# Kernel tuning notes

Hardware: AMD Instinct MI355X
Metric: run time of the kernel (lower is better)

Reference implementation:

```python
import jax, jax.numpy as jnp
from jax import lax
import numpy as np

B, QLEN, HQ, HKV, D, MAXLEN = 16, 1, 32, 8, 128, 8192
END_INDEX = 4096


def setup_inputs() -> dict:
    key = jax.random.key(0)
    k1, k2, k3, k4, k5 = jax.random.split(key, 5)
    query = jax.random.normal(k1, (B, QLEN, HQ, D), dtype=jnp.float32)
    new_key = jax.random.normal(k2, (B, QLEN, HKV, D), dtype=jnp.float32)
    new_value = jax.random.normal(k3, (B, QLEN, HKV, D), dtype=jnp.float32)
    key_cache = jax.random.normal(k4, (B, MAXLEN, HKV, D), dtype=jnp.float32)
    value_cache = jax.random.normal(k5, (B, MAXLEN, HKV, D), dtype=jnp.float32)
    attention_mask = jnp.ones((B, MAXLEN), dtype=jnp.bool_)
    # standard lower-triangular causal mask, (1, 1, L, L)
    causal_mask = jnp.tril(jnp.ones((MAXLEN, MAXLEN), dtype=jnp.bool_))[None, None]
    return {
        "query": query,
        "key": new_key,
        "value": new_value,
        "key_cache": key_cache,
        "value_cache": value_cache,
        "attention_mask": attention_mask,
        "causal_mask": causal_mask,
        "end_index": END_INDEX,
    }


def reference(query, key, value, key_cache, value_cache, attention_mask, causal_mask, end_index):
    # Faithful translation of FlaxAttentionModule._concatenate_to_cache + bias
    # construction in `concatenate` (decode path with a cache_view).
    num_updated = query.shape[1]              # q_len
    max_length = value_cache.shape[1]
    dtype = query.dtype

    # attention_mask: (B, L) -> (B, 1, 1, L)
    mask = attention_mask[:, None, None, :]

    # causal mask slice at the current write position: (1,1,q_len,L)
    cm = lax.dynamic_slice(causal_mask, (0, 0, end_index, 0), (1, 1, num_updated, max_length))
    cm = jnp.broadcast_to(cm, (query.shape[0],) + cm.shape[1:])
    mask = jnp.logical_and(jnp.broadcast_to(mask, cm.shape), cm)

    # scatter the new key/value into the ring-buffer cache
    slice_indices = (0, end_index % max_length, 0, 0)
    value_cache = lax.dynamic_update_slice(value_cache, value, slice_indices)
    key_cache = lax.dynamic_update_slice(key_cache, key, slice_indices)

    # pad mask: positions beyond the filled prefix are invalid
    pad_mask = jnp.broadcast_to(
        jnp.arange(max_length) < end_index + num_updated,
        (query.shape[0], 1, num_updated, max_length),
    )
    mask = jnp.logical_and(pad_mask, mask)

    # attention bias: 0 where attended, finfo.min where masked
    attention_bias = jnp.where(
        mask,
        jnp.zeros((), dtype),
        jnp.full((), jnp.finfo(dtype).min, dtype),
    )
    return key_cache, value_cache, mask, attention_bias
```

## Files before the change

### kernel.cpp

```cpp
#include <hip/hip_runtime.h>
#include <float.h>

#define BATCH   16
#define MAXLEN  8192
#define HKV     8
#define HDIM    128
#define ROWF    (HKV * HDIM)
#define ROW4    (ROWF / 4)
#define CACHE_F (BATCH * MAXLEN * ROWF)
#define CACHE_4 (CACHE_F / 4)
#define NMASK   (BATCH * MAXLEN)
#define NFIX    (2 * BATCH * ROW4)

typedef float v4f __attribute__((ext_vector_type(4)));

__global__ void fixup_mask_bias(const v4f* __restrict__ new_key,
                                const v4f* __restrict__ new_value,
                                const unsigned char* __restrict__ attn_mask,
                                const unsigned char* __restrict__ causal_mask,
                                const int* __restrict__ end_index_p,
                                v4f* __restrict__ out4,
                                float* __restrict__ mask_out,
                                float* __restrict__ bias_out) {
    const int i = blockIdx.x * blockDim.x + threadIdx.x;
    const int end = *end_index_p;
    const int upd_s = end % MAXLEN;

    if (i < NFIX) {
        const int half = i / (BATCH * ROW4);
        const int b    = (i / ROW4) % BATCH;
        const int r    = i % ROW4;
        const v4f* src = half ? new_value : new_key;
        const long long dst = (long long)half * CACHE_4
                            + ((long long)b * MAXLEN + upd_s) * ROW4 + r;
        out4[dst] = src[b * ROW4 + r];
    }

    if (i < NMASK) {
        const int j = i % MAXLEN;
        const bool am  = attn_mask[i] != 0;
        const bool cm  = causal_mask[(long long)end * MAXLEN + j] != 0;
        const bool pad = j < (end + 1);
        const bool m = am && cm && pad;
        const float neg_big = __uint_as_float(0xFF7F0000u);
        mask_out[i] = m ? 1.0f : 0.0f;
        bias_out[i] = m ? 0.0f : neg_big;
    }
}

extern "C" void kernel_launch(void* const* d_in, const int* in_sizes, int n_in,
                              void* d_out, int out_size, void* d_ws, size_t ws_size,
                              hipStream_t stream) {
    const v4f* new_key     = (const v4f*)d_in[1];
    const v4f* new_value   = (const v4f*)d_in[2];
    const unsigned char* attn_mask   = (const unsigned char*)d_in[5];
    const unsigned char* causal_mask = (const unsigned char*)d_in[6];
    const int* end_index_p    = (const int*)d_in[7];

    float* out = (float*)d_out;
    float* mask_out = out + 2LL * CACHE_F;
    float* bias_out = mask_out + NMASK;

    hipMemcpyAsync(out,            d_in[3], (size_t)CACHE_F * sizeof(float),
                   hipMemcpyDeviceToDevice, stream);
    hipMemcpyAsync(out + CACHE_F,  d_in[4], (size_t)CACHE_F * sizeof(float),
                   hipMemcpyDeviceToDevice, stream);

    fixup_mask_bias<<<(NMASK + 255) / 256, 256, 0, stream>>>(
        new_key, new_value, attn_mask, causal_mask, end_index_p,
        (v4f*)d_out, mask_out, bias_out);
}
```

Before: 411.5 us.

## Fuse cache copies, new-row scatter and mask generation into one kernel

Replaces the two device-to-device memcpys and the fixup kernel with a single grid-stride kernel. It copies both caches using nontemporal vector loads and stores, substituting the new key/value rows inline, and writes the mask and bias vectorized by four. This removes the separate launches and the double write of the updated row. Its performance depends on the custom copy loop matching the bandwidth of the runtime's blit copy.

```diff
diff --git a/kernel.cpp b/kernel.cpp
--- a/kernel.cpp
+++ b/kernel.cpp
@@ -1,5 +1,4 @@
 #include <hip/hip_runtime.h>
-#include <float.h>
 
 #define BATCH   16
 #define MAXLEN  8192
@@ -10,41 +9,61 @@
 #define CACHE_F (BATCH * MAXLEN * ROWF)
 #define CACHE_4 (CACHE_F / 4)
 #define NMASK   (BATCH * MAXLEN)
-#define NFIX    (2 * BATCH * ROW4)
+#define TOTAL4  (2 * CACHE_4)
 
 typedef float v4f __attribute__((ext_vector_type(4)));
 
-__global__ void fixup_mask_bias(const v4f* __restrict__ new_key,
-                                const v4f* __restrict__ new_value,
-                                const unsigned char* __restrict__ attn_mask,
-                                const unsigned char* __restrict__ causal_mask,
-                                const int* __restrict__ end_index_p,
-                                v4f* __restrict__ out4,
-                                float* __restrict__ mask_out,
-                                float* __restrict__ bias_out) {
-    const int i = blockIdx.x * blockDim.x + threadIdx.x;
-    const int end = *end_index_p;
-    const int upd_s = end % MAXLEN;
+__global__ __launch_bounds__(256) void fused_copy_fixup_mask(
+    const v4f* __restrict__ key_cache,
+    const v4f* __restrict__ value_cache,
+    const v4f* __restrict__ new_key,
+    const v4f* __restrict__ new_value,
+    const unsigned char* __restrict__ attn_mask,
+    const unsigned char* __restrict__ causal_mask,
+    const int* __restrict__ end_index_p,
+    v4f* __restrict__ out4,
+    float* __restrict__ mask_out,
+    float* __restrict__ bias_out)
+{
+    const int tid      = blockIdx.x * blockDim.x + threadIdx.x;
+    const int nthreads = gridDim.x * blockDim.x;
+    const int end      = *end_index_p;
+    const int upd_s    = end & (MAXLEN - 1);
 
-    if (i < NFIX) {
-        const int half = i / (BATCH * ROW4);
-        const int b    = (i / ROW4) % BATCH;
-        const int r    = i % ROW4;
-        const v4f* src = half ? new_value : new_key;
-        const long long dst = (long long)half * CACHE_4
-                            + ((long long)b * MAXLEN + upd_s) * ROW4 + r;
-        out4[dst] = src[b * ROW4 + r];
+    if (tid < NMASK / 4) {
+        const int j0 = (tid * 4) & (MAXLEN - 1);
+        const uchar4 am = *(const uchar4*)(attn_mask + tid * 4);
+        const uchar4 cm = *(const uchar4*)(causal_mask
+                              + (long long)end * MAXLEN + j0);
+        const float neg_big = __uint_as_float(0xFF7F0000u);
+        const unsigned char amv[4] = {am.x, am.y, am.z, am.w};
+        const unsigned char cmv[4] = {cm.x, cm.y, cm.z, cm.w};
+        v4f m, bs;
+        #pragma unroll
+        for (int k = 0; k < 4; ++k) {
+            const bool mm = amv[k] && cmv[k] && ((j0 + k) < (end + 1));
+            m[k]  = mm ? 1.0f : 0.0f;
+            bs[k] = mm ? 0.0f : neg_big;
+        }
+        *(v4f*)(mask_out + tid * 4) = m;
+        *(v4f*)(bias_out + tid * 4) = bs;
     }
 
-    if (i < NMASK) {
-        const int j = i % MAXLEN;
-        const bool am  = attn_mask[i] != 0;
-        const bool cm  = causal_mask[(long long)end * MAXLEN + j] != 0;
-        const bool pad = j < (end + 1);
-        const bool m = am && cm && pad;
-        const float neg_big = __uint_as_float(0xFF7F0000u);
-        mask_out[i] = m ? 1.0f : 0.0f;
-        bias_out[i] = m ? 0.0f : neg_big;
+    for (int idx = tid; idx < TOTAL4; idx += nthreads) {
+        const int half   = idx >> 25;
+        const int within = idx & (CACHE_4 - 1);
+        const int row    = within >> 8;
+        const int s      = row & (MAXLEN - 1);
+        v4f val;
+        if (s == upd_s) {
+            const int b = row >> 13;
+            const int r = within & (ROW4 - 1);
+            val = (half ? new_value : new_key)[b * ROW4 + r];
+        } else {
+            val = __builtin_nontemporal_load(
+                (half ? value_cache : key_cache) + within);
+        }
+        __builtin_nontemporal_store(val, out4 + idx);
     }
 }
 
@@ -53,20 +72,18 @@
                               hipStream_t stream) {
     const v4f* new_key     = (const v4f*)d_in[1];
     const v4f* new_value   = (const v4f*)d_in[2];
+    const v4f* key_cache   = (const v4f*)d_in[3];
+    const v4f* value_cache = (const v4f*)d_in[4];
     const unsigned char* attn_mask   = (const unsigned char*)d_in[5];
     const unsigned char* causal_mask = (const unsigned char*)d_in[6];
-    const int* end_index_p    = (const int*)d_in[7];
+    const int* end_index_p = (const int*)d_in[7];
 
-    float* out = (float*)d_out;
+    float* out      = (float*)d_out;
     float* mask_out = out + 2LL * CACHE_F;
     float* bias_out = mask_out + NMASK;
 
-    hipMemcpyAsync(out,            d_in[3], (size_t)CACHE_F * sizeof(float),
-                   hipMemcpyDeviceToDevice, stream);
-    hipMemcpyAsync(out + CACHE_F,  d_in[4], (size_t)CACHE_F * sizeof(float),
-                   hipMemcpyDeviceToDevice, stream);
-
-    fixup_mask_bias<<<(NMASK + 255) / 256, 256, 0, stream>>>(
-        new_key, new_value, attn_mask, causal_mask, end_index_p,
+    fused_copy_fixup_mask<<<2048, 256, 0, stream>>>(
+        key_cache, value_cache, new_key, new_value,
+        attn_mask, causal_mask, end_index_p,
         (v4f*)d_out, mask_out, bias_out);
 }
```

Result: slower. 440.7 us (+7.1%).
